# Optimization experiments

Hardware: AMD Instinct MI355X
Metric: run time of the kernel (lower is better)

## Reference

```python
import jax, jax.numpy as jnp
import numpy as np

N_ATOMS = 50000
N_EDGES = 640000
D = 128
N_RBF = 20
N_INTER = 3

act = jax.nn.softplus


def setup_inputs() -> dict:
    key = jax.random.key(0)
    ks = jax.random.split(key, 16)
    s = 1.0 / np.sqrt(D)
    inp = {
        "x": jax.random.normal(ks[0], (N_ATOMS, D), jnp.float32),
        "g_ij": jax.random.uniform(ks[1], (N_EDGES, N_RBF), jnp.float32),
        "idx_i": jax.random.randint(ks[2], (N_EDGES,), 0, N_ATOMS),
        "idx_j": jax.random.randint(ks[3], (N_EDGES,), 0, N_ATOMS),
        "n_atoms": N_ATOMS,
        "u": jnp.ones((D,), jnp.float32),
        "Wf": jax.random.normal(ks[4], (D, D), jnp.float32) * s,
        "bf": jnp.zeros((D,), jnp.float32),
        # linear_g weight init to zero in original; use small random so grads flow
        "Wg": jax.random.normal(ks[5], (D, N_RBF), jnp.float32) * 0.01,
        "bg": jnp.zeros((D,), jnp.float32),
        "Wj": jax.random.normal(ks[6], (D, D), jnp.float32) * s,
        "bj": jnp.zeros((D,), jnp.float32),
        "Wi": jax.random.normal(ks[7], (D, D), jnp.float32) * s,
        "bi": jnp.zeros((D,), jnp.float32),
        "res_w1": jax.random.normal(ks[8], (N_INTER, D, D), jnp.float32) * s,
        "res_b1": jnp.zeros((N_INTER, D), jnp.float32),
        "res_w2": jax.random.normal(ks[9], (N_INTER, D, D), jnp.float32) * s,
        "res_b2": jnp.zeros((N_INTER, D), jnp.float32),
    }
    return inp


def reference(x, g_ij, idx_i, idx_j, n_atoms, u, Wf, bf, Wg, bg, Wj, bj, Wi, bi,
              res_w1, res_b1, res_w2, res_b2):
    x_j = x[idx_j]                                    # [E, D] gather
    xp = u * x                                        # [N, D]
    # sequential_j: act -> linear_j -> act, gated by linear_g(g_ij)
    vp = act(act(x_j) @ Wj.T + bj) * (g_ij @ Wg.T + bg)   # [E, D]
    vm = act(act(x) @ Wi.T + bi)                      # [N, D]
    v = jax.ops.segment_sum(vp, idx_i, num_segments=n_atoms) + vm
    for l in range(res_w1.shape[0]):
        h = act(v) @ res_w1[l].T + res_b1[l]
        h = act(h) @ res_w2[l].T + res_b2[l]
        v = h + v
    v = act(v)
    return xp + v @ Wf.T + bf
```

## Files before the change

kernel.cpp:

```cpp
#include <hip/hip_runtime.h>
#include <hip/hip_fp16.h>

#define DD 128

typedef __attribute__((ext_vector_type(8))) short short8;
typedef __attribute__((ext_vector_type(8))) unsigned short ushort8;
typedef __attribute__((ext_vector_type(4))) float floatx4;
typedef unsigned int uint32;

__device__ __forceinline__ float sp(float x) {
    return fmaxf(x, 0.0f) + __logf(1.0f + __expf(-fabsf(x)));
}

__device__ __forceinline__ unsigned short f2bf(float f) {
    union { float f; uint32 u; } c; c.f = f;
    const uint32 u = c.u;
    return (unsigned short)((u + 0x7fffu + ((u >> 16) & 1u)) >> 16);
}

__device__ __forceinline__ unsigned short f2h(float f) {
    __half h = __float2half(f);
    return __builtin_bit_cast(unsigned short, h);
}

__global__ __launch_bounds__(256)
void convert_w(const float* __restrict__ Wj, const float* __restrict__ Wi,
               const float* __restrict__ rw1, const float* __restrict__ rw2,
               const float* __restrict__ Wf, unsigned short* __restrict__ out,
               const float* __restrict__ g, unsigned short* __restrict__ gh,
               int gchunks)
{
    if ((int)blockIdx.x >= 72) {
        const int gid = ((int)blockIdx.x - 72) * 256 + threadIdx.x;
        if (gid < gchunks) {
            const float4 f0 = reinterpret_cast<const float4*>(g)[2 * gid];
            const float4 f1 = reinterpret_cast<const float4*>(g)[2 * gid + 1];
            ushort8 o;
            o[0] = f2h(f0.x); o[1] = f2h(f0.y); o[2] = f2h(f0.z); o[3] = f2h(f0.w);
            o[4] = f2h(f1.x); o[5] = f2h(f1.y); o[6] = f2h(f1.z); o[7] = f2h(f1.w);
            reinterpret_cast<ushort8*>(gh)[gid] = o;
        }
        return;
    }
    const int gid = blockIdx.x * 256 + threadIdx.x;
    const int mat = gid >> 11;
    const int r   = gid & 2047;
    const int ln  = r & 63;
    const int ntkk = r >> 6;
    const float* src;
    if      (mat == 0) src = Wj;
    else if (mat == 1) src = Wi;
    else if (mat <= 4) src = rw1 + (size_t)(mat - 2) * 16384;
    else if (mat <= 7) src = rw2 + (size_t)(mat - 5) * 16384;
    else               src = Wf;
    const int row = (ntkk >> 2) * 16 + (ln & 15);
    const int c0  = ((ntkk & 3) * 4 + (ln >> 4)) * 8;
    const float* s = src + row * DD + c0;
    const float4 a = *reinterpret_cast<const float4*>(s);
    const float4 b = *reinterpret_cast<const float4*>(s + 4);
    ushort8 u8;
    u8[0] = f2bf(a.x); u8[1] = f2bf(a.y); u8[2] = f2bf(a.z); u8[3] = f2bf(a.w);
    u8[4] = f2bf(b.x); u8[5] = f2bf(b.y); u8[6] = f2bf(b.z); u8[7] = f2bf(b.w);
    *reinterpret_cast<ushort8*>(out + (size_t)mat * 16384 + (size_t)r * 8) = u8;
}

__device__ __forceinline__ void stage_wb(const unsigned short* __restrict__ Wb,
                                         unsigned short* wl, int t)
{
    #pragma unroll
    for (int i = 0; i < 8; ++i) {
        const int c = t + i * 256;
        *reinterpret_cast<ushort8*>(wl + c * 8) =
            *reinterpret_cast<const ushort8*>(Wb + c * 8);
    }
}

__device__ __forceinline__ void load_afrag_act(const float* __restrict__ X,
                                               int m, int q, int n, short8 af[4])
{
    const int mm = m < n ? m : n - 1;
    const float* row = X + (size_t)mm * DD + q * 8;
    #pragma unroll
    for (int kk = 0; kk < 4; ++kk) {
        const float4 a = *reinterpret_cast<const float4*>(row + kk * 32);
        const float4 b = *reinterpret_cast<const float4*>(row + kk * 32 + 4);
        ushort8 u;
        u[0] = f2bf(sp(a.x)); u[1] = f2bf(sp(a.y)); u[2] = f2bf(sp(a.z)); u[3] = f2bf(sp(a.w));
        u[4] = f2bf(sp(b.x)); u[5] = f2bf(sp(b.y)); u[6] = f2bf(sp(b.z)); u[7] = f2bf(sp(b.w));
        af[kk] = __builtin_bit_cast(short8, u);
    }
}

__device__ __forceinline__ void mfma_gemm(const unsigned short* __restrict__ wsrc,
                                          const short8 af[4], int lane, floatx4 acc[8])
{
    #pragma unroll
    for (int nt = 0; nt < 8; ++nt) {
        #pragma unroll
        for (int kk = 0; kk < 4; ++kk) {
            const short8 bfr = *reinterpret_cast<const short8*>(
                wsrc + (size_t)(((nt * 4 + kk) << 6) + lane) * 8);
            acc[nt] = __builtin_amdgcn_mfma_f32_16x16x32_bf16(af[kk], bfr, acc[nt], 0, 0, 0);
        }
    }
}

__global__ __launch_bounds__(256, 4)
void dual_gemm(const float* __restrict__ x,
               const unsigned short* __restrict__ Wb,
               const float* __restrict__ bj, const float* __restrict__ bi,
               unsigned short* __restrict__ Aout, float* __restrict__ vout, int n)
{
    __shared__ __align__(16) unsigned short wl[128 * 128];
    const int t = threadIdx.x;
    const int lane = t & 63, wv = t >> 6;
    const int cl = lane & 15, q = lane >> 4;
    const int m0 = blockIdx.x * 64 + wv * 16;

    short8 af[4];
    load_afrag_act(x, m0 + cl, q, n, af);

    stage_wb(Wb, wl, t);
    __syncthreads();

    floatx4 acc[8];
    #pragma unroll
    for (int nt = 0; nt < 8; ++nt) acc[nt] = (floatx4){0.f, 0.f, 0.f, 0.f};
    mfma_gemm(wl, af, lane, acc);

    #pragma unroll
    for (int nt = 0; nt < 8; ++nt) {
        const int col = nt * 16 + cl;
        const float bb = bj[col];
        #pragma unroll
        for (int r = 0; r < 4; ++r) {
            const int row = m0 + q * 4 + r;
            if (row < n) Aout[(size_t)row * DD + col] = f2bf(sp(acc[nt][r] + bb));
        }
    }

    __syncthreads();
    stage_wb(Wb + 16384, wl, t);
    __syncthreads();

    #pragma unroll
    for (int nt = 0; nt < 8; ++nt) acc[nt] = (floatx4){0.f, 0.f, 0.f, 0.f};
    mfma_gemm(wl, af, lane, acc);

    #pragma unroll
    for (int nt = 0; nt < 8; ++nt) {
        const int col = nt * 16 + cl;
        const float bb = bi[col];
        #pragma unroll
        for (int r = 0; r < 4; ++r) {
            const int row = m0 + q * 4 + r;
            if (row < n) vout[(size_t)row * DD + col] = sp(acc[nt][r] + bb);
        }
    }
}

__global__ __launch_bounds__(256, 4)
void tail_kernel(const float* __restrict__ vin, const float* __restrict__ x,
                 const unsigned short* __restrict__ Wb,
                 const float* __restrict__ rb1, const float* __restrict__ rb2,
                 const float* __restrict__ bf, const float* __restrict__ u,
                 float* __restrict__ out, int n)
{
    __shared__ __align__(16) unsigned short hl[64 * 128];
    const int t = threadIdx.x;
    const int lane = t & 63, wv = t >> 6;
    const int cl = lane & 15, q = lane >> 4;
    const int mb = blockIdx.x * 64;
    const int ml2 = wv * 16 + cl;

    floatx4 vac[8];
    #pragma unroll
    for (int nt = 0; nt < 8; ++nt) {
        #pragma unroll
        for (int r = 0; r < 4; ++r) {
            const int row = mb + wv * 16 + q * 4 + r;
            const int col = nt * 16 + cl;
            vac[nt][r] = (row < n) ? vin[(size_t)row * DD + col] : 0.f;
        }
    }

    short8 af[4];
    load_afrag_act(vin, mb + wv * 16 + cl, q, n, af);

    #pragma unroll
    for (int l = 0; l < 3; ++l) {
        const unsigned short* W1 = Wb + (size_t)(2 + l) * 16384;
        const unsigned short* W2 = Wb + (size_t)(5 + l) * 16384;

        if (l > 0) {
            #pragma unroll
            for (int nt = 0; nt < 8; ++nt) {
                const int col = nt * 16 + cl;
                const int ch = col >> 3;
                #pragma unroll
                for (int r = 0; r < 4; ++r) {
                    const int ml = wv * 16 + q * 4 + r;
                    hl[ml * 128 + ((ch ^ (ml & 15)) << 3) + (col & 7)] = f2bf(sp(vac[nt][r]));
                }
            }
            #pragma unroll
            for (int kk = 0; kk < 4; ++kk)
                af[kk] = *reinterpret_cast<const short8*>(hl + ml2 * 128 + (((kk * 4 + q) ^ cl) << 3));
        }

        floatx4 acc[8];
        #pragma unroll
        for (int nt = 0; nt < 8; ++nt) acc[nt] = (floatx4){0.f, 0.f, 0.f, 0.f};
        mfma_gemm(W1, af, lane, acc);

        const float* b1 = rb1 + (size_t)l * DD;
        #pragma unroll
        for (int nt = 0; nt < 8; ++nt) {
            const int col = nt * 16 + cl;
            const int ch = col >> 3;
            const float bb = b1[col];
            #pragma unroll
            for (int r = 0; r < 4; ++r) {
                const int ml = wv * 16 + q * 4 + r;
                hl[ml * 128 + ((ch ^ (ml & 15)) << 3) + (col & 7)] = f2bf(sp(acc[nt][r] + bb));
            }
        }
        short8 af2[4];
        #pragma unroll
        for (int kk = 0; kk < 4; ++kk)
            af2[kk] = *reinterpret_cast<const short8*>(hl + ml2 * 128 + (((kk * 4 + q) ^ cl) << 3));

        mfma_gemm(W2, af2, lane, vac);
        const float* b2 = rb2 + (size_t)l * DD;
        #pragma unroll
        for (int nt = 0; nt < 8; ++nt) {
            const float bb = b2[nt * 16 + cl];
            #pragma unroll
            for (int r = 0; r < 4; ++r) vac[nt][r] += bb;
        }
    }

    #pragma unroll
    for (int nt = 0; nt < 8; ++nt) {
        const int col = nt * 16 + cl;
        const int ch = col >> 3;
        #pragma unroll
        for (int r = 0; r < 4; ++r) {
            const int ml = wv * 16 + q * 4 + r;
            hl[ml * 128 + ((ch ^ (ml & 15)) << 3) + (col & 7)] = f2bf(sp(vac[nt][r]));
        }
    }
    short8 aff[4];
    #pragma unroll
    for (int kk = 0; kk < 4; ++kk)
        aff[kk] = *reinterpret_cast<const short8*>(hl + ml2 * 128 + (((kk * 4 + q) ^ cl) << 3));

    floatx4 acc[8];
    #pragma unroll
    for (int nt = 0; nt < 8; ++nt) acc[nt] = (floatx4){0.f, 0.f, 0.f, 0.f};
    mfma_gemm(Wb + (size_t)8 * 16384, aff, lane, acc);

    #pragma unroll
    for (int nt = 0; nt < 8; ++nt) {
        const int col = nt * 16 + cl;
        const float bb = bf[col];
        const float uu = u[col];
        #pragma unroll
        for (int r = 0; r < 4; ++r) {
            const int row = mb + wv * 16 + q * 4 + r;
            if (row < n)
                out[(size_t)row * DD + col] =
                    acc[nt][r] + bb + uu * x[(size_t)row * DD + col];
        }
    }
}


__global__ __launch_bounds__(256)
void hist_kernel(const int* __restrict__ idx_i, int* __restrict__ cnt, int E)
{
    const int e = blockIdx.x * 256 + threadIdx.x;
    if (e < E) atomicAdd(&cnt[idx_i[e]], 1);
}

__global__ __launch_bounds__(256)
void scan_reduce(const int* __restrict__ cnt, int* __restrict__ bsum, int n)
{
    __shared__ int wsum[4];
    const int t = threadIdx.x;
    const int lane = t & 63, wv = t >> 6;
    const int i0 = blockIdx.x * 1024 + t * 4;
    int s = 0;
    #pragma unroll
    for (int k = 0; k < 4; ++k) if (i0 + k < n) s += cnt[i0 + k];
    #pragma unroll
    for (int d = 1; d < 64; d <<= 1) s += __shfl_down(s, d, 64);
    if (lane == 0) wsum[wv] = s;
    __syncthreads();
    if (t == 0) bsum[blockIdx.x] = wsum[0] + wsum[1] + wsum[2] + wsum[3];
}

__global__ __launch_bounds__(256)
void scan_apply(const int* __restrict__ cnt, const int* __restrict__ bsum,
                int* __restrict__ off, int* __restrict__ cnt2, int n, int nb)
{
    __shared__ int wsum[4];
    const int t = threadIdx.x;
    const int lane = t & 63, wv = t >> 6;

    int bval = (lane < nb && lane < (int)blockIdx.x) ? bsum[lane] : 0;
    #pragma unroll
    for (int d = 32; d >= 1; d >>= 1) bval += __shfl_down(bval, d, 64);
    const int blk_off = __shfl(bval, 0, 64);

    const int i0 = blockIdx.x * 1024 + t * 4;
    const int v0 = (i0 + 0 < n) ? cnt[i0 + 0] : 0;
    const int v1 = (i0 + 1 < n) ? cnt[i0 + 1] : 0;
    const int v2 = (i0 + 2 < n) ? cnt[i0 + 2] : 0;
    const int v3 = (i0 + 3 < n) ? cnt[i0 + 3] : 0;
    const int s = v0 + v1 + v2 + v3;
    int incl = s;
    #pragma unroll
    for (int d = 1; d < 64; d <<= 1) {
        const int y = __shfl_up(incl, d, 64);
        if (lane >= d) incl += y;
    }
    if (lane == 63) wsum[wv] = incl;
    __syncthreads();
    int woff = blk_off;
    #pragma unroll
    for (int w = 0; w < 4; ++w) if (w < wv) woff += wsum[w];
    const int excl = woff + incl - s;
    if (i0 + 0 < n) { off[i0 + 0] = excl;                cnt2[i0 + 0] = 0; }
    if (i0 + 1 < n) { off[i0 + 1] = excl + v0;           cnt2[i0 + 1] = 0; }
    if (i0 + 2 < n) { off[i0 + 2] = excl + v0 + v1;      cnt2[i0 + 2] = 0; }
    if (i0 + 3 < n) { off[i0 + 3] = excl + v0 + v1 + v2; cnt2[i0 + 3] = 0; }
}

__global__ __launch_bounds__(256)
void scatter_kernel(const int* __restrict__ idx_i, const int* __restrict__ idx_j,
                    const int* __restrict__ off, int* __restrict__ cnt2,
                    int2* __restrict__ spair, int E)
{
    const int e = blockIdx.x * 256 + threadIdx.x;
    if (e < E) {
        const int i = idx_i[e];
        const int p = off[i] + atomicAdd(&cnt2[i], 1);
        spair[p] = make_int2(e, idx_j[e]);
    }
}

template<int GH>
__global__ __launch_bounds__(256, 4)
void agg_kernel(const int* __restrict__ off, const int* __restrict__ cnt,
                const int2* __restrict__ spair,
                const unsigned short* __restrict__ gh,
                const float* __restrict__ g,
                const float* __restrict__ Wg, const float* __restrict__ bg,
                const unsigned short* __restrict__ A, float* __restrict__ v, int N)
{
    const int t = threadIdx.x;
    const int lane = t & 63;
    const int wid0 = blockIdx.x * 4 + (t >> 6);
    const int nw   = gridDim.x * 4;
    const int d0 = lane << 1;

    const float bg0 = bg[d0], bg1 = bg[d0 + 1];

    if (GH) {
        __half2 w0h[10], w1h[10];
        #pragma unroll
        for (int k2 = 0; k2 < 10; ++k2) {
            w0h[k2] = __floats2half2_rn(Wg[d0 * 20 + 2 * k2], Wg[d0 * 20 + 2 * k2 + 1]);
            w1h[k2] = __floats2half2_rn(Wg[(d0 + 1) * 20 + 2 * k2], Wg[(d0 + 1) * 20 + 2 * k2 + 1]);
        }

        for (int i = wid0; i < N; i += nw) {
            const int beg = off[i], num = cnt[i], end = beg + num;
            float2 acc = *reinterpret_cast<const float2*>(v + (size_t)i * DD + d0);

            int p = beg;
            while (p + 4 <= end) {
                int ee[4], jj[4];
                #pragma unroll
                for (int u = 0; u < 4; ++u) {
                    const int2 pr = spair[p + u];
                    ee[u] = __builtin_amdgcn_readfirstlane(pr.x);
                    jj[u] = __builtin_amdgcn_readfirstlane(pr.y);
                }
                uint32 aa[4];
                float2 gq[4][5];
                #pragma unroll
                for (int u = 0; u < 4; ++u) {
                    aa[u] = *reinterpret_cast<const uint32*>(A + (size_t)jj[u] * DD + d0);
                    const float2* gp = reinterpret_cast<const float2*>(gh + (size_t)ee[u] * 20);
                    #pragma unroll
                    for (int q2 = 0; q2 < 5; ++q2) gq[u][q2] = gp[q2];
                }
                #pragma unroll
                for (int u = 0; u < 4; ++u) {
                    __half2 a0 = __float2half2_rn(0.f), a1 = __float2half2_rn(0.f);
                    #pragma unroll
                    for (int q2 = 0; q2 < 5; ++q2) {
                        const __half2 h0 = __builtin_bit_cast(__half2, gq[u][q2].x);
                        const __half2 h1 = __builtin_bit_cast(__half2, gq[u][q2].y);
                        a0 = __hfma2(h0, w0h[2 * q2], a0);
                        a1 = __hfma2(h0, w1h[2 * q2], a1);
                        a0 = __hfma2(h1, w0h[2 * q2 + 1], a0);
                        a1 = __hfma2(h1, w1h[2 * q2 + 1], a1);
                    }
                    const float t0 = bg0 + __low2float(a0) + __high2float(a0);
                    const float t1 = bg1 + __low2float(a1) + __high2float(a1);
                    union { uint32 u32; float f; } cx, cy;
                    cx.u32 = aa[u] << 16;
                    cy.u32 = aa[u] & 0xffff0000u;
                    acc.x = fmaf(cx.f, t0, acc.x);
                    acc.y = fmaf(cy.f, t1, acc.y);
                }
                p += 4;
            }
            for (; p < end; ++p) {
                const int2 pr = spair[p];
                const int e0 = __builtin_amdgcn_readfirstlane(pr.x);
                const int j0 = __builtin_amdgcn_readfirstlane(pr.y);
                const uint32 a0u = *reinterpret_cast<const uint32*>(A + (size_t)j0 * DD + d0);
                const float2* gp = reinterpret_cast<const float2*>(gh + (size_t)e0 * 20);
                __half2 a0 = __float2half2_rn(0.f), a1 = __float2half2_rn(0.f);
                #pragma unroll
                for (int q2 = 0; q2 < 5; ++q2) {
                    const float2 qq = gp[q2];
                    const __half2 h0 = __builtin_bit_cast(__half2, qq.x);
                    const __half2 h1 = __builtin_bit_cast(__half2, qq.y);
                    a0 = __hfma2(h0, w0h[2 * q2], a0);
                    a1 = __hfma2(h0, w1h[2 * q2], a1);
                    a0 = __hfma2(h1, w0h[2 * q2 + 1], a0);
                    a1 = __hfma2(h1, w1h[2 * q2 + 1], a1);
                }
                const float t0 = bg0 + __low2float(a0) + __high2float(a0);
                const float t1 = bg1 + __low2float(a1) + __high2float(a1);
                union { uint32 u32; float f; } cx, cy;
                cx.u32 = a0u << 16;
                cy.u32 = a0u & 0xffff0000u;
                acc.x = fmaf(cx.f, t0, acc.x);
                acc.y = fmaf(cy.f, t1, acc.y);
            }
            *reinterpret_cast<float2*>(v + (size_t)i * DD + d0) = acc;
        }
    } else {
        float2 wg01[20];
        #pragma unroll
        for (int k = 0; k < 20; ++k) {
            wg01[k].x = Wg[d0 * 20 + k];
            wg01[k].y = Wg[(d0 + 1) * 20 + k];
        }
        for (int i = wid0; i < N; i += nw) {
            const int beg = off[i], num = cnt[i], end = beg + num;
            float2 acc = *reinterpret_cast<const float2*>(v + (size_t)i * DD + d0);
            int p = beg;
            for (; p + 2 <= end; p += 2) {
                const int2 pr0 = spair[p];
                const int2 pr1 = spair[p + 1];
                const int e0 = __builtin_amdgcn_readfirstlane(pr0.x);
                const int j0 = __builtin_amdgcn_readfirstlane(pr0.y);
                const int e1 = __builtin_amdgcn_readfirstlane(pr1.x);
                const int j1 = __builtin_amdgcn_readfirstlane(pr1.y);
                const uint32 a0 = *reinterpret_cast<const uint32*>(A + (size_t)j0 * DD + d0);
                const uint32 a1 = *reinterpret_cast<const uint32*>(A + (size_t)j1 * DD + d0);
                const float4* g0p = reinterpret_cast<const float4*>(g + (size_t)e0 * 20);
                const float4* g1p = reinterpret_cast<const float4*>(g + (size_t)e1 * 20);
                float2 t0 = make_float2(bg0, bg1), t1 = make_float2(bg0, bg1);
                #pragma unroll
                for (int qq = 0; qq < 5; ++qq) {
                    const float4 p0 = g0p[qq];
                    const float4 p1 = g1p[qq];
                    t0.x = fmaf(p0.x, wg01[qq*4+0].x, t0.x); t0.y = fmaf(p0.x, wg01[qq*4+0].y, t0.y);
                    t0.x = fmaf(p0.y, wg01[qq*4+1].x, t0.x); t0.y = fmaf(p0.y, wg01[qq*4+1].y, t0.y);
                    t0.x = fmaf(p0.z, wg01[qq*4+2].x, t0.x); t0.y = fmaf(p0.z, wg01[qq*4+2].y, t0.y);
                    t0.x = fmaf(p0.w, wg01[qq*4+3].x, t0.x); t0.y = fmaf(p0.w, wg01[qq*4+3].y, t0.y);
                    t1.x = fmaf(p1.x, wg01[qq*4+0].x, t1.x); t1.y = fmaf(p1.x, wg01[qq*4+0].y, t1.y);
                    t1.x = fmaf(p1.y, wg01[qq*4+1].x, t1.x); t1.y = fmaf(p1.y, wg01[qq*4+1].y, t1.y);
                    t1.x = fmaf(p1.z, wg01[qq*4+2].x, t1.x); t1.y = fmaf(p1.z, wg01[qq*4+2].y, t1.y);
                    t1.x = fmaf(p1.w, wg01[qq*4+3].x, t1.x); t1.y = fmaf(p1.w, wg01[qq*4+3].y, t1.y);
                }
                union { uint32 u; float f; } c0x, c0y, c1x, c1y;
                c0x.u = a0 << 16; c0y.u = a0 & 0xffff0000u;
                c1x.u = a1 << 16; c1y.u = a1 & 0xffff0000u;
                acc.x = fmaf(c0x.f, t0.x, acc.x); acc.y = fmaf(c0y.f, t0.y, acc.y);
                acc.x = fmaf(c1x.f, t1.x, acc.x); acc.y = fmaf(c1y.f, t1.y, acc.y);
            }
            if (p < end) {
                const int2 pr0 = spair[p];
                const int e0 = __builtin_amdgcn_readfirstlane(pr0.x);
                const int j0 = __builtin_amdgcn_readfirstlane(pr0.y);
                const uint32 a0 = *reinterpret_cast<const uint32*>(A + (size_t)j0 * DD + d0);
                const float4* g0p = reinterpret_cast<const float4*>(g + (size_t)e0 * 20);
                float2 t0 = make_float2(bg0, bg1);
                #pragma unroll
                for (int qq = 0; qq < 5; ++qq) {
                    const float4 p0 = g0p[qq];
                    t0.x = fmaf(p0.x, wg01[qq*4+0].x, t0.x); t0.y = fmaf(p0.x, wg01[qq*4+0].y, t0.y);
                    t0.x = fmaf(p0.y, wg01[qq*4+1].x, t0.x); t0.y = fmaf(p0.y, wg01[qq*4+1].y, t0.y);
                    t0.x = fmaf(p0.z, wg01[qq*4+2].x, t0.x); t0.y = fmaf(p0.z, wg01[qq*4+2].y, t0.y);
                    t0.x = fmaf(p0.w, wg01[qq*4+3].x, t0.x); t0.y = fmaf(p0.w, wg01[qq*4+3].y, t0.y);
                }
                union { uint32 u; float f; } c0x, c0y;
                c0x.u = a0 << 16; c0y.u = a0 & 0xffff0000u;
                acc.x = fmaf(c0x.f, t0.x, acc.x); acc.y = fmaf(c0y.f, t0.y, acc.y);
            }
            *reinterpret_cast<float2*>(v + (size_t)i * DD + d0) = acc;
        }
    }
}

extern "C" void kernel_launch(void* const* d_in, const int* in_sizes, int n_in,
                              void* d_out, int out_size, void* d_ws, size_t ws_size,
                              hipStream_t stream)
{
    const float* x     = (const float*)d_in[0];
    const float* g     = (const float*)d_in[1];
    const int*   idx_i = (const int*)d_in[2];
    const int*   idx_j = (const int*)d_in[3];
    const float* u     = (const float*)d_in[5];
    const float* Wf    = (const float*)d_in[6];
    const float* bf    = (const float*)d_in[7];
    const float* Wg    = (const float*)d_in[8];
    const float* bg    = (const float*)d_in[9];
    const float* Wj    = (const float*)d_in[10];
    const float* bj    = (const float*)d_in[11];
    const float* Wi    = (const float*)d_in[12];
    const float* bi    = (const float*)d_in[13];
    const float* rw1   = (const float*)d_in[14];
    const float* rb1   = (const float*)d_in[15];
    const float* rw2   = (const float*)d_in[16];
    const float* rb2   = (const float*)d_in[17];

    const int N = in_sizes[0] / DD;
    const int E = in_sizes[2];
    float* out = (float*)d_out;

    float*          v     = (float*)d_ws;
    unsigned short* A     = (unsigned short*)(v + (size_t)N * DD);
    int*            cnt   = (int*)(A + (size_t)N * DD);
    int*            off   = cnt + N;
    int*            cnt2  = off + N;
    int*            bsum  = cnt2 + N;
    int2*           spair = (int2*)(bsum + 64);
    unsigned short* Wb    = (unsigned short*)(spair + E);
    unsigned short* gh    = Wb + 9 * 16384;

    const size_t need_gh = (size_t)((char*)(gh + (size_t)E * 20) - (char*)d_ws);
    const bool gh_ok = ws_size >= need_gh;

    dim3 blk(256);
    const int tiles    = (N + 63) / 64;
    const int eblocks  = (E + 255) / 256;
    const int sblocks  = (N + 1023) / 1024;
    const int gchunks  = gh_ok ? (E * 20) / 8 : 0;
    const int gblocks  = gh_ok ? (gchunks + 255) / 256 : 0;

    convert_w<<<72 + gblocks, blk, 0, stream>>>(Wj, Wi, rw1, rw2, Wf, Wb,
                                                g, gh, gchunks);

    hipMemsetAsync(cnt, 0, (size_t)N * sizeof(int), stream);
    hist_kernel<<<eblocks, blk, 0, stream>>>(idx_i, cnt, E);
    scan_reduce<<<sblocks, blk, 0, stream>>>(cnt, bsum, N);
    scan_apply<<<sblocks, blk, 0, stream>>>(cnt, bsum, off, cnt2, N, sblocks);
    scatter_kernel<<<eblocks, blk, 0, stream>>>(idx_i, idx_j, off, cnt2, spair, E);

    dual_gemm<<<tiles, blk, 0, stream>>>(x, Wb, bj, bi, A, v, N);

    if (gh_ok)
        agg_kernel<1><<<2048, blk, 0, stream>>>(off, cnt, spair, gh, g,
                                                Wg, bg, A, v, N);
    else
        agg_kernel<0><<<2048, blk, 0, stream>>>(off, cnt, spair, gh, g,
                                                Wg, bg, A, v, N);

    tail_kernel<<<tiles, blk, 0, stream>>>(v, x, Wb, rb1, rb2, bf, u, out, N);
}
```

Baseline: 257.9 us.

## Stage tail-kernel weights in LDS and double block size to 512 threads

The tail kernel now uses 512-thread blocks covering 128 rows and copies each 128x128 bf16 weight matrix into shared memory before its MFMA GEMM, instead of reading weights straight from global memory per wave. This shares each weight load across 8 waves and removes repeated global/L2 weight traffic. In exchange it adds barriers around every staging step, serialises staging with compute, and uses 64KB of LDS per block, which may lower occupancy.

```diff
diff --git a/kernel.cpp b/kernel.cpp
--- a/kernel.cpp
+++ b/kernel.cpp
@@ -75,6 +75,17 @@
     }
 }
 
+__device__ __forceinline__ void stage_wb512(const unsigned short* __restrict__ Wb,
+                                            unsigned short* wl, int t)
+{
+    #pragma unroll
+    for (int i = 0; i < 4; ++i) {
+        const int c = t + i * 512;
+        *reinterpret_cast<ushort8*>(wl + c * 8) =
+            *reinterpret_cast<const ushort8*>(Wb + c * 8);
+    }
+}
+
 __device__ __forceinline__ void load_afrag_act(const float* __restrict__ X,
                                                int m, int q, int n, short8 af[4])
 {
@@ -159,18 +170,19 @@
     }
 }
 
-__global__ __launch_bounds__(256, 4)
+__global__ __launch_bounds__(512, 4)
 void tail_kernel(const float* __restrict__ vin, const float* __restrict__ x,
                  const unsigned short* __restrict__ Wb,
                  const float* __restrict__ rb1, const float* __restrict__ rb2,
                  const float* __restrict__ bf, const float* __restrict__ u,
                  float* __restrict__ out, int n)
 {
-    __shared__ __align__(16) unsigned short hl[64 * 128];
+    __shared__ __align__(16) unsigned short wl[128 * 128];
+    __shared__ __align__(16) unsigned short hl[128 * 128];
     const int t = threadIdx.x;
     const int lane = t & 63, wv = t >> 6;
     const int cl = lane & 15, q = lane >> 4;
-    const int mb = blockIdx.x * 64;
+    const int mb = blockIdx.x * 128;
     const int ml2 = wv * 16 + cl;
 
     floatx4 vac[8];
@@ -187,11 +199,11 @@
     short8 af[4];
     load_afrag_act(vin, mb + wv * 16 + cl, q, n, af);
 
+    stage_wb512(Wb + 2 * 16384, wl, t);
+    __syncthreads();
+
     #pragma unroll
     for (int l = 0; l < 3; ++l) {
-        const unsigned short* W1 = Wb + (size_t)(2 + l) * 16384;
-        const unsigned short* W2 = Wb + (size_t)(5 + l) * 16384;
-
         if (l > 0) {
             #pragma unroll
             for (int nt = 0; nt < 8; ++nt) {
@@ -211,7 +223,7 @@
         floatx4 acc[8];
         #pragma unroll
         for (int nt = 0; nt < 8; ++nt) acc[nt] = (floatx4){0.f, 0.f, 0.f, 0.f};
-        mfma_gemm(W1, af, lane, acc);
+        mfma_gemm(wl, af, lane, acc);
 
         const float* b1 = rb1 + (size_t)l * DD;
         #pragma unroll
@@ -230,7 +242,11 @@
         for (int kk = 0; kk < 4; ++kk)
             af2[kk] = *reinterpret_cast<const short8*>(hl + ml2 * 128 + (((kk * 4 + q) ^ cl) << 3));
 
-        mfma_gemm(W2, af2, lane, vac);
+        __syncthreads();
+        stage_wb512(Wb + (size_t)(5 + l) * 16384, wl, t);
+        __syncthreads();
+
+        mfma_gemm(wl, af2, lane, vac);
         const float* b2 = rb2 + (size_t)l * DD;
         #pragma unroll
         for (int nt = 0; nt < 8; ++nt) {
@@ -238,6 +254,11 @@
             #pragma unroll
             for (int r = 0; r < 4; ++r) vac[nt][r] += bb;
         }
+
+        __syncthreads();
+        const int nxt = (l < 2) ? (3 + l) : 8;
+        stage_wb512(Wb + (size_t)nxt * 16384, wl, t);
+        __syncthreads();
     }
 
     #pragma unroll
@@ -258,7 +279,7 @@
     floatx4 acc[8];
     #pragma unroll
     for (int nt = 0; nt < 8; ++nt) acc[nt] = (floatx4){0.f, 0.f, 0.f, 0.f};
-    mfma_gemm(Wb + (size_t)8 * 16384, aff, lane, acc);
+    mfma_gemm(wl, aff, lane, acc);
 
     #pragma unroll
     for (int nt = 0; nt < 8; ++nt) {
@@ -553,6 +574,7 @@
 
     dim3 blk(256);
     const int tiles    = (N + 63) / 64;
+    const int ttiles   = (N + 127) / 128;
     const int eblocks  = (E + 255) / 256;
     const int sblocks  = (N + 1023) / 1024;
     const int gchunks  = gh_ok ? (E * 20) / 8 : 0;
@@ -576,5 +598,5 @@
         agg_kernel<0><<<2048, blk, 0, stream>>>(off, cnt, spair, gh, g,
                                                 Wg, bg, A, v, N);
 
-    tail_kernel<<<tiles, blk, 0, stream>>>(v, x, Wb, rb1, rb2, bf, u, out, N);
-}
+    tail_kernel<<<ttiles, dim3(512), 0, stream>>>(v, x, Wb, rb1, rb2, bf, u, out, N);
+}
```

After: 244.7 us. 5.1% less time.

## Fuse histogram into prep kernel with ranks, merge scatter into dual GEMM launch

Applied to the files above, without the earlier changes.

The histogram atomics now record each edge's rank within its segment, so the scatter step no longer needs a second atomic pass or the zeroed cnt2 array. The histogram is folded into the weight/g conversion launch, and the scatter is merged with the dual GEMM launch so independent work shares one grid. This cuts the number of kernel launches and the serialization between small kernels. It adds an E-sized rank buffer to the workspace, and the tail kernel's occupancy hint is lowered from 4 to 3 blocks per CU.

```diff
diff --git a/kernel.cpp b/kernel.cpp
--- a/kernel.cpp
+++ b/kernel.cpp
@@ -24,14 +24,22 @@
 }
 
 __global__ __launch_bounds__(256)
-void convert_w(const float* __restrict__ Wj, const float* __restrict__ Wi,
-               const float* __restrict__ rw1, const float* __restrict__ rw2,
-               const float* __restrict__ Wf, unsigned short* __restrict__ out,
-               const float* __restrict__ g, unsigned short* __restrict__ gh,
-               int gchunks)
-{
-    if ((int)blockIdx.x >= 72) {
-        const int gid = ((int)blockIdx.x - 72) * 256 + threadIdx.x;
+void prep_kernel(const float* __restrict__ Wj, const float* __restrict__ Wi,
+                 const float* __restrict__ rw1, const float* __restrict__ rw2,
+                 const float* __restrict__ Wf, unsigned short* __restrict__ out,
+                 const float* __restrict__ g, unsigned short* __restrict__ gh,
+                 int gchunks, int gh_blocks,
+                 const int* __restrict__ idx_i, int* __restrict__ cnt,
+                 int* __restrict__ rank, int E)
+{
+    const int b = (int)blockIdx.x;
+    if (b >= 72 + gh_blocks) {
+        const int e = (b - 72 - gh_blocks) * 256 + threadIdx.x;
+        if (e < E) rank[e] = atomicAdd(&cnt[idx_i[e]], 1);
+        return;
+    }
+    if (b >= 72) {
+        const int gid = (b - 72) * 256 + threadIdx.x;
         if (gid < gchunks) {
             const float4 f0 = reinterpret_cast<const float4*>(g)[2 * gid];
             const float4 f1 = reinterpret_cast<const float4*>(g)[2 * gid + 1];
@@ -42,7 +50,7 @@
         }
         return;
     }
-    const int gid = blockIdx.x * 256 + threadIdx.x;
+    const int gid = b * 256 + threadIdx.x;
     const int mat = gid >> 11;
     const int r   = gid & 2047;
     const int ln  = r & 63;
@@ -57,10 +65,10 @@
     const int c0  = ((ntkk & 3) * 4 + (ln >> 4)) * 8;
     const float* s = src + row * DD + c0;
     const float4 a = *reinterpret_cast<const float4*>(s);
-    const float4 b = *reinterpret_cast<const float4*>(s + 4);
+    const float4 bb = *reinterpret_cast<const float4*>(s + 4);
     ushort8 u8;
     u8[0] = f2bf(a.x); u8[1] = f2bf(a.y); u8[2] = f2bf(a.z); u8[3] = f2bf(a.w);
-    u8[4] = f2bf(b.x); u8[5] = f2bf(b.y); u8[6] = f2bf(b.z); u8[7] = f2bf(b.w);
+    u8[4] = f2bf(bb.x); u8[5] = f2bf(bb.y); u8[6] = f2bf(bb.z); u8[7] = f2bf(bb.w);
     *reinterpret_cast<ushort8*>(out + (size_t)mat * 16384 + (size_t)r * 8) = u8;
 }
 
@@ -106,16 +114,31 @@
 }
 
 __global__ __launch_bounds__(256, 4)
-void dual_gemm(const float* __restrict__ x,
-               const unsigned short* __restrict__ Wb,
-               const float* __restrict__ bj, const float* __restrict__ bi,
-               unsigned short* __restrict__ Aout, float* __restrict__ vout, int n)
+void scatter_dual(const int* __restrict__ idx_i, const int* __restrict__ idx_j,
+                  const int* __restrict__ off, const int* __restrict__ rank,
+                  int2* __restrict__ spair, int E, int eblocks,
+                  const float* __restrict__ x,
+                  const unsigned short* __restrict__ Wb,
+                  const float* __restrict__ bj, const float* __restrict__ bi,
+                  unsigned short* __restrict__ Aout, float* __restrict__ vout, int n)
 {
     __shared__ __align__(16) unsigned short wl[128 * 128];
     const int t = threadIdx.x;
+
+    if ((int)blockIdx.x < eblocks) {
+        const int e = blockIdx.x * 256 + t;
+        if (e < E) {
+            const int i = idx_i[e];
+            const int p = off[i] + rank[e];
+            spair[p] = make_int2(e, idx_j[e]);
+        }
+        return;
+    }
+
+    const int bid = (int)blockIdx.x - eblocks;
     const int lane = t & 63, wv = t >> 6;
     const int cl = lane & 15, q = lane >> 4;
-    const int m0 = blockIdx.x * 64 + wv * 16;
+    const int m0 = bid * 64 + wv * 16;
 
     short8 af[4];
     load_afrag_act(x, m0 + cl, q, n, af);
@@ -159,7 +182,7 @@
     }
 }
 
-__global__ __launch_bounds__(256, 4)
+__global__ __launch_bounds__(256, 3)
 void tail_kernel(const float* __restrict__ vin, const float* __restrict__ x,
                  const unsigned short* __restrict__ Wb,
                  const float* __restrict__ rb1, const float* __restrict__ rb2,
@@ -277,13 +300,6 @@
 
 
 __global__ __launch_bounds__(256)
-void hist_kernel(const int* __restrict__ idx_i, int* __restrict__ cnt, int E)
-{
-    const int e = blockIdx.x * 256 + threadIdx.x;
-    if (e < E) atomicAdd(&cnt[idx_i[e]], 1);
-}
-
-__global__ __launch_bounds__(256)
 void scan_reduce(const int* __restrict__ cnt, int* __restrict__ bsum, int n)
 {
     __shared__ int wsum[4];
@@ -302,7 +318,7 @@
 
 __global__ __launch_bounds__(256)
 void scan_apply(const int* __restrict__ cnt, const int* __restrict__ bsum,
-                int* __restrict__ off, int* __restrict__ cnt2, int n, int nb)
+                int* __restrict__ off, int n, int nb)
 {
     __shared__ int wsum[4];
     const int t = threadIdx.x;
@@ -331,23 +347,10 @@
     #pragma unroll
     for (int w = 0; w < 4; ++w) if (w < wv) woff += wsum[w];
     const int excl = woff + incl - s;
-    if (i0 + 0 < n) { off[i0 + 0] = excl;                cnt2[i0 + 0] = 0; }
-    if (i0 + 1 < n) { off[i0 + 1] = excl + v0;           cnt2[i0 + 1] = 0; }
-    if (i0 + 2 < n) { off[i0 + 2] = excl + v0 + v1;      cnt2[i0 + 2] = 0; }
-    if (i0 + 3 < n) { off[i0 + 3] = excl + v0 + v1 + v2; cnt2[i0 + 3] = 0; }
-}
-
-__global__ __launch_bounds__(256)
-void scatter_kernel(const int* __restrict__ idx_i, const int* __restrict__ idx_j,
-                    const int* __restrict__ off, int* __restrict__ cnt2,
-                    int2* __restrict__ spair, int E)
-{
-    const int e = blockIdx.x * 256 + threadIdx.x;
-    if (e < E) {
-        const int i = idx_i[e];
-        const int p = off[i] + atomicAdd(&cnt2[i], 1);
-        spair[p] = make_int2(e, idx_j[e]);
-    }
+    if (i0 + 0 < n) off[i0 + 0] = excl;
+    if (i0 + 1 < n) off[i0 + 1] = excl + v0;
+    if (i0 + 2 < n) off[i0 + 2] = excl + v0 + v1;
+    if (i0 + 3 < n) off[i0 + 3] = excl + v0 + v1 + v2;
 }
 
 template<int GH>
@@ -542,9 +545,9 @@
     unsigned short* A     = (unsigned short*)(v + (size_t)N * DD);
     int*            cnt   = (int*)(A + (size_t)N * DD);
     int*            off   = cnt + N;
-    int*            cnt2  = off + N;
-    int*            bsum  = cnt2 + N;
-    int2*           spair = (int2*)(bsum + 64);
+    int*            bsum  = off + N;
+    int*            rank  = bsum + 64;
+    int2*           spair = (int2*)(rank + E);
     unsigned short* Wb    = (unsigned short*)(spair + E);
     unsigned short* gh    = Wb + 9 * 16384;
 
@@ -558,16 +561,17 @@
     const int gchunks  = gh_ok ? (E * 20) / 8 : 0;
     const int gblocks  = gh_ok ? (gchunks + 255) / 256 : 0;
 
-    convert_w<<<72 + gblocks, blk, 0, stream>>>(Wj, Wi, rw1, rw2, Wf, Wb,
-                                                g, gh, gchunks);
-
     hipMemsetAsync(cnt, 0, (size_t)N * sizeof(int), stream);
-    hist_kernel<<<eblocks, blk, 0, stream>>>(idx_i, cnt, E);
+
+    prep_kernel<<<72 + gblocks + eblocks, blk, 0, stream>>>(
+        Wj, Wi, rw1, rw2, Wf, Wb, g, gh, gchunks, gblocks, idx_i, cnt, rank, E);
+
     scan_reduce<<<sblocks, blk, 0, stream>>>(cnt, bsum, N);
-    scan_apply<<<sblocks, blk, 0, stream>>>(cnt, bsum, off, cnt2, N, sblocks);
-    scatter_kernel<<<eblocks, blk, 0, stream>>>(idx_i, idx_j, off, cnt2, spair, E);
-
-    dual_gemm<<<tiles, blk, 0, stream>>>(x, Wb, bj, bi, A, v, N);
+    scan_apply<<<sblocks, blk, 0, stream>>>(cnt, bsum, off, N, sblocks);
+
+    scatter_dual<<<eblocks + tiles, blk, 0, stream>>>(
+        idx_i, idx_j, off, rank, spair, E, eblocks,
+        x, Wb, bj, bi, A, v, N);
 
     if (gh_ok)
         agg_kernel<1><<<2048, blk, 0, stream>>>(off, cnt, spair, gh, g,
```

Measured after the change: 256.4 us (median of 2 runs). About the same (-0.6%).
